# Kernel optimization log

Hardware: AMD Instinct MI355X
Metric: run time of the kernel (lower is better)

Reference implementation:

```python
import jax, jax.numpy as jnp
import numpy as np

B, T, C = 2, 192, 512
H, D = 8, 64  # num_heads, head_dim; inner_dim = H*D = C


def setup_inputs() -> dict:
    key = jax.random.key(0)
    k1, k2, k3 = jax.random.split(key, 3)
    x = jax.random.normal(k1, (B, T, C), dtype=jnp.float32)
    W_in = jax.random.normal(k2, (C, 5 * H * D), dtype=jnp.float32) * 0.02
    b_in = jnp.zeros((5 * H * D,), dtype=jnp.float32)
    W_out = jax.random.normal(k3, (H * D, C), dtype=jnp.float32) * 0.02
    b_out = jnp.zeros((C,), dtype=jnp.float32)
    return {"x": x, "W_in": W_in, "b_in": b_in, "W_out": W_out, "b_out": b_out}


def _split_heads(t):
    # (B,T,H*D) -> (B,H,T,D)
    return t.reshape(B, T, H, D).transpose(0, 2, 1, 3)


def reference(x, W_in, b_in, W_out, b_out):
    scale = D ** -0.5
    proj = x @ W_in + b_in  # (B,T,5*H*D)
    q, k1, v1, k2, v2 = jnp.split(proj, 5, axis=-1)
    q = _split_heads(q) * scale
    k1 = _split_heads(k1)
    v1 = _split_heads(v1)
    k2 = _split_heads(k2)
    v2 = _split_heads(v2)
    # trilinear logits: <q_i, k1_j, k2_k> / sqrt(D), computed in fp32
    logits = jnp.einsum('bhid,bhjd,bhkd->bhijk', q, k1, k2,
                        preferred_element_type=jnp.float32)
    # softmax over the joint (j,k) axes
    attn = jax.nn.softmax(logits.reshape(B, H, T, T * T), axis=-1)
    attn = attn.reshape(B, H, T, T, T).astype(x.dtype)
    # out_i[d] = sum_{j,k} attn[i,j,k] * v1_j[d] * v2_k[d]
    out = jnp.einsum('bhijk,bhjd,bhkd->bhid', attn, v1, v2)
    y = out.transpose(0, 2, 1, 3).reshape(B, T, H * D)  # merge heads
    return y @ W_out + b_out
```

## Files before the change

### kernel.cpp

```cpp
#include <hip/hip_runtime.h>
#include <hip/hip_bf16.h>


typedef float  v4f __attribute__((ext_vector_type(4)));
typedef short  v8s __attribute__((ext_vector_type(8)));

__device__ __forceinline__ unsigned short f2bf(float f) {
  unsigned u = __float_as_uint(f);
  u += 0x7fffu + ((u >> 16) & 1u);
  return (unsigned short)(u >> 16);
}
__device__ __forceinline__ float bf2f(unsigned short b) {
  return __uint_as_float(((unsigned)b) << 16);
}
__device__ __forceinline__ unsigned pack_bf16(float lo, float hi) {
  __hip_bfloat162 t = __float22bfloat162_rn(float2{lo, hi});
  union { __hip_bfloat162 b; unsigned u; } cv;
  cv.b = t;
  return cv.u;
}

#if __has_builtin(__builtin_amdgcn_exp2f)
#define EXP2F(x) __builtin_amdgcn_exp2f(x)
#else
#define EXP2F(x) exp2f(x)
#endif

#define MFMA32(a, b, c) __builtin_amdgcn_mfma_f32_16x16x32_bf16((a), (b), (c), 0, 0, 0)

#define QSCALE 0.18033688011112042f


#define XH_OFF   589824
#define XL_OFF   786432
#define WTH_OFF  983040
#define WTL_OFF  2293760
#define WOTH_OFF 3604480
#define WOTL_OFF 3866624
#define OH_OFF   4128768
#define OL_OFF   4325376

__device__ __forceinline__ int v1perm(int t) {
  return (t & ~31) | (((t >> 2) & 3) << 3) | ((t & 3) << 1) | ((t >> 4) & 1);
}

__global__ __launch_bounds__(256) void prep_kernel(
    const float* __restrict__ x, const float* __restrict__ Win,
    const float* __restrict__ Wout, unsigned short* __restrict__ wsh) {
  __shared__ float tile[32 * 65];
  const int bi = blockIdx.x, t = threadIdx.x;
  if (bi < 768) {
    const float* W; unsigned short *Th, *Tl; int R, n0, k0;
    if (bi < 640) {
      W = Win; Th = wsh + WTH_OFF; Tl = wsh + WTL_OFF; R = 2560;
      n0 = (bi % 40) << 6; k0 = (bi / 40) << 5;
    } else {
      const int idx = bi - 640;
      W = Wout; Th = wsh + WOTH_OFF; Tl = wsh + WOTL_OFF; R = 512;
      n0 = (idx & 7) << 6; k0 = (idx >> 3) << 5;
    }
    const int n = t & 63, kq = (t >> 6) * 8;
#pragma unroll
    for (int j = 0; j < 8; ++j)
      tile[(kq + j) * 65 + n] = W[(k0 + kq + j) * R + n0 + n];
    __syncthreads();
    const int n2 = t >> 2, ks = (t & 3) * 8;
    union { uint4 u; unsigned short us[8]; } ph, pl;
#pragma unroll
    for (int j = 0; j < 8; ++j) {
      const float v = tile[(ks + j) * 65 + n2];
      const unsigned short h = f2bf(v);
      ph.us[j] = h;
      pl.us[j] = f2bf(v - bf2f(h));
    }
    *(uint4*)(Th + (n0 + n2) * 512 + k0 + ks) = ph.u;
    *(uint4*)(Tl + (n0 + n2) * 512 + k0 + ks) = pl.u;
  } else {
    const int flat = ((bi - 768) * 256 + t) * 8;
    const v4f v0 = *(const v4f*)(x + flat);
    const v4f v1 = *(const v4f*)(x + flat + 4);
    union { uint4 u; unsigned short us[8]; } ph, pl;
#pragma unroll
    for (int j = 0; j < 4; ++j) {
      unsigned short h = f2bf(v0[j]);
      ph.us[j] = h; pl.us[j] = f2bf(v0[j] - bf2f(h));
      h = f2bf(v1[j]);
      ph.us[4 + j] = h; pl.us[4 + j] = f2bf(v1[j] - bf2f(h));
    }
    *(uint4*)(wsh + XH_OFF + flat) = ph.u;
    *(uint4*)(wsh + XL_OFF + flat) = pl.u;
  }
}

__global__ __launch_bounds__(64) void proj_kernel(
    const unsigned short* __restrict__ wsh, const float* __restrict__ bin,
    float* __restrict__ wsf, unsigned short* __restrict__ wshd) {
  const int lane = threadIdx.x;
  const int c = lane & 15, q = lane >> 4;
  const int bm = blockIdx.x % 12, bn = blockIdx.x / 12;

  const unsigned short* base[8];
  base[0] = wsh + XH_OFF + (bm * 32 + c) * 512 + (q << 3);
  base[1] = base[0] + 16 * 512;
  base[2] = wsh + XL_OFF + (bm * 32 + c) * 512 + (q << 3);
  base[3] = base[2] + 16 * 512;
  base[4] = wsh + WTH_OFF + (bn * 32 + c) * 512 + (q << 3);
  base[5] = base[4] + 16 * 512;
  base[6] = wsh + WTL_OFF + (bn * 32 + c) * 512 + (q << 3);
  base[7] = base[6] + 16 * 512;

  const v4f z = {0.f, 0.f, 0.f, 0.f};
  v4f a00 = z, a01 = z, a10 = z, a11 = z;

  v8s cur[8], nxt[8];
#pragma unroll
  for (int i = 0; i < 8; ++i) cur[i] = *(const v8s*)(base[i]);
#pragma unroll
  for (int i = 0; i < 8; ++i) nxt[i] = *(const v8s*)(base[i] + 32);

#pragma unroll 1
  for (int ks = 0; ks < 16; ++ks) {
    v8s nx2[8];
    if (ks < 14) {
      const int o = (ks + 2) * 32;
#pragma unroll
      for (int i = 0; i < 8; ++i) nx2[i] = *(const v8s*)(base[i] + o);
    }
    a00 = MFMA32(cur[2], cur[4], a00); a00 = MFMA32(cur[0], cur[6], a00); a00 = MFMA32(cur[0], cur[4], a00);
    a01 = MFMA32(cur[2], cur[5], a01); a01 = MFMA32(cur[0], cur[7], a01); a01 = MFMA32(cur[0], cur[5], a01);
    a10 = MFMA32(cur[3], cur[4], a10); a10 = MFMA32(cur[1], cur[6], a10); a10 = MFMA32(cur[1], cur[4], a10);
    a11 = MFMA32(cur[3], cur[5], a11); a11 = MFMA32(cur[1], cur[7], a11); a11 = MFMA32(cur[1], cur[5], a11);
#pragma unroll
    for (int i = 0; i < 8; ++i) { cur[i] = nxt[i]; nxt[i] = nx2[i]; }
  }

  v4f accs[2][2] = {{a00, a01}, {a10, a11}};
#pragma unroll
  for (int mt = 0; mt < 2; ++mt) {
#pragma unroll
    for (int nt = 0; nt < 2; ++nt) {
      const int n = bn * 32 + nt * 16 + c;
      const int which = n >> 9, cc = n & 511, h = cc >> 6, d = cc & 63;
      const float bv = bin[n];
#pragma unroll
      for (int r = 0; r < 4; ++r) {
        const int m = bm * 32 + mt * 16 + (q << 2) + r;
        const int b = (m >= 192) ? 1 : 0;
        const int tt = m - (b ? 192 : 0);
        const int bh = b * 8 + h;
        const float val = accs[mt][nt][r] + bv;
        const int rm = ((bh * 192 + tt) << 6) + d;
        if (which == 0)      wsf[rm] = val * QSCALE;
        else if (which == 1) wshd[rm] = f2bf(val);
        else if (which == 2) wshd[393216 + ((bh << 6) + d) * 192 + v1perm(tt)] = f2bf(val);
        else if (which == 3) wshd[196608 + rm] = f2bf(val);
        else wsf[196608 + ((bh * 192 + tt) * 16 + (d & 15)) * 4 + (d >> 4)] = val;
      }
    }
  }
}

__global__ __launch_bounds__(256, 2) void attn_kernel(
    const float* __restrict__ wsf, const unsigned short* __restrict__ wsh,
    float* __restrict__ accp, float* __restrict__ Sp) {
  __shared__ char smem[16640];
  unsigned short* K2s = (unsigned short*)smem;

  const int tid  = threadIdx.x;
  const int wv   = tid >> 6;
  const int lane = tid & 63;
  const int c    = lane & 15;
  const int quad = lane >> 4;
  const int jh   = wv & 1;
  const int kh   = wv >> 1;

  const int bb = blockIdx.x;
  const int kb = bb & 3;
  const int it = (bb >> 2) % 12;
  const int bh = bb / 48;

  const unsigned short* k1g = wsh + bh * 192 * 64;
  const unsigned short* v1g = wsh + 393216 + bh * 64 * 192;
  const unsigned short* k2g = wsh + 196608 + bh * 192 * 64;
  const float*          v2g = wsf + 196608 + bh * 12288;

  for (int idx = tid; idx < 384; idx += 256) {
    const int r = idx >> 3, c8 = (idx & 7) * 8;
    *(uint4*)(K2s + r * 64 + c8) = *(const uint4*)(k2g + (kb * 48 + r) * 64 + c8);
  }

  v8s k1f[6][2];
#pragma unroll
  for (int j = 0; j < 6; ++j) {
    const unsigned short* kp = k1g + (((jh * 6 + j) * 16 + c) << 6) + (quad << 3);
    k1f[j][0] = *(const v8s*)(kp);
    k1f[j][1] = *(const v8s*)(kp + 32);
  }

  v8s vf[3][4];
#pragma unroll
  for (int m = 0; m < 3; ++m)
#pragma unroll
    for (int t = 0; t < 4; ++t)
      vf[m][t] = *(const v8s*)(v1g + (c + 16 * t) * 192 + ((jh * 3 + m) << 5) + (quad << 3));

  const float* qg = wsf + ((bh * 192 + it * 16 + c) << 6) + (quad << 3);
  float q0[8], q1[8];
  {
    v4f qa = *(const v4f*)(qg), qb = *(const v4f*)(qg + 4);
    v4f qc = *(const v4f*)(qg + 32), qd = *(const v4f*)(qg + 36);
#pragma unroll
    for (int e = 0; e < 4; ++e) {
      q0[e] = qa[e]; q0[4 + e] = qb[e];
      q1[e] = qc[e]; q1[4 + e] = qd[e];
    }
  }
  __syncthreads();

  unsigned* Pw = (unsigned*)(smem + 6144) + wv * 320;
  const v4f z = {0.f, 0.f, 0.f, 0.f};
  v4f acc[4] = {z, z, z, z};
  v4f oS = z;
  const short one = (short)0x3F80;
  const v8s ones = {one, one, one, one, one, one, one, one};

  union U4 { uint4 u4; unsigned short us[8]; };
  union AF { v8s v; unsigned u[4]; };

#pragma unroll 1
  for (int ks = 0; ks < 24; ++ks) {
    const int rl = kh * 24 + ks;
    U4 kl, khh;
    kl.u4  = *(const uint4*)(K2s + (rl << 6) + (quad << 3));
    khh.u4 = *(const uint4*)(K2s + (rl << 6) + (quad << 3) + 32);
    const v4f v2v = *(const v4f*)(v2g + (((kb * 48 + rl) << 4) + c) * 4);

    AF af0, af1;
#pragma unroll
    for (int e = 0; e < 4; ++e) {
      af0.u[e] = pack_bf16(q0[2*e] * bf2f(kl.us[2*e]),  q0[2*e+1] * bf2f(kl.us[2*e+1]));
      af1.u[e] = pack_bf16(q1[2*e] * bf2f(khh.us[2*e]), q1[2*e+1] * bf2f(khh.us[2*e+1]));
    }

    v4f o0 = z, o1 = z, o2 = z, o3 = z;
#pragma unroll
    for (int m = 0; m < 3; ++m) {
      v4f Ca = MFMA32(af0.v, k1f[2*m][0], z);
      Ca = MFMA32(af1.v, k1f[2*m][1], Ca);
      v4f Cb = MFMA32(af0.v, k1f[2*m+1][0], z);
      Cb = MFMA32(af1.v, k1f[2*m+1][1], Cb);
#pragma unroll
      for (int r = 0; r < 4; ++r) { Ca[r] = EXP2F(Ca[r]); Cb[r] = EXP2F(Cb[r]); }
#pragma unroll
      for (int r = 0; r < 4; ++r)
        Pw[((quad << 2) + r) * 20 + c] = pack_bf16(Ca[r], Cb[r]);
      const v8s ap = *(const v8s*)(Pw + c * 20 + (quad << 2));
      oS = MFMA32(ap, ones, oS);
      o0 = MFMA32(ap, vf[m][0], o0);
      o1 = MFMA32(ap, vf[m][1], o1);
      o2 = MFMA32(ap, vf[m][2], o2);
      o3 = MFMA32(ap, vf[m][3], o3);
    }
    acc[0] += o0 * v2v[0];
    acc[1] += o1 * v2v[1];
    acc[2] += o2 * v2v[2];
    acc[3] += o3 * v2v[3];
  }

  __syncthreads();
  float* redA = (float*)smem;
  float* redS = (float*)smem + 4096;

  if (c == 0) {
    float* rs = redS + wv * 16 + (quad << 2);
#pragma unroll
    for (int r = 0; r < 4; ++r) rs[r] = oS[r];
  }
#pragma unroll
  for (int r = 0; r < 4; ++r) {
    float* rr = redA + wv * 1024 + (((quad << 2) + r) << 6) + c;
    rr[0] = acc[0][r]; rr[16] = acc[1][r]; rr[32] = acc[2][r]; rr[48] = acc[3][r];
  }
  __syncthreads();

  const int pbase = (bh * 12 + it) * 4 + kb;
  float* ap_out = accp + pbase * 1024;
  for (int idx = tid; idx < 1024; idx += 256)
    ap_out[idx] = redA[idx] + redA[1024 + idx] + redA[2048 + idx] + redA[3072 + idx];
  if (tid < 16)
    Sp[pbase * 16 + tid] = redS[tid] + redS[16 + tid] + redS[32 + tid] + redS[48 + tid];
}

__global__ __launch_bounds__(256) void norm_kernel(
    const float* __restrict__ accp, const float* __restrict__ Sp,
    unsigned short* __restrict__ wsh) {
  const int flat = blockIdx.x * 2048 + threadIdx.x * 8;
  const int m = flat >> 9, cc = flat & 511;
  const int b = (m >= 192) ? 1 : 0;
  const int tt = m - (b ? 192 : 0);
  const int h = cc >> 6, d0 = cc & 63;
  const int bh = b * 8 + h, it = tt >> 4, i = tt & 15;
  const int pb = (bh * 12 + it) * 4;
  const float* ap = accp + pb * 1024 + (i << 6) + d0;
  v4f a0 = *(const v4f*)(ap), a1 = *(const v4f*)(ap + 4);
  float Sv = Sp[pb * 16 + i];
#pragma unroll
  for (int kb = 1; kb < 4; ++kb) {
    a0 += *(const v4f*)(ap + kb * 1024);
    a1 += *(const v4f*)(ap + kb * 1024 + 4);
    Sv += Sp[(pb + kb) * 16 + i];
  }
  const float inv = 1.0f / Sv;
  union { uint4 u; unsigned short us[8]; } ph, pl;
#pragma unroll
  for (int j = 0; j < 4; ++j) {
    float v = a0[j] * inv;
    unsigned short hh = f2bf(v);
    ph.us[j] = hh; pl.us[j] = f2bf(v - bf2f(hh));
    v = a1[j] * inv;
    hh = f2bf(v);
    ph.us[4 + j] = hh; pl.us[4 + j] = f2bf(v - bf2f(hh));
  }
  *(uint4*)(wsh + OH_OFF + flat) = ph.u;
  *(uint4*)(wsh + OL_OFF + flat) = pl.u;
}

__global__ __launch_bounds__(64) void outp_kernel(
    const unsigned short* __restrict__ wsh, const float* __restrict__ bout,
    float* __restrict__ y) {
  const int lane = threadIdx.x;
  const int c = lane & 15, q = lane >> 4;
  const int bm = blockIdx.x % 12, bn = blockIdx.x / 12;

  const unsigned short* base[8];
  base[0] = wsh + OH_OFF + (bm * 32 + c) * 512 + (q << 3);
  base[1] = base[0] + 16 * 512;
  base[2] = wsh + OL_OFF + (bm * 32 + c) * 512 + (q << 3);
  base[3] = base[2] + 16 * 512;
  base[4] = wsh + WOTH_OFF + (bn * 32 + c) * 512 + (q << 3);
  base[5] = base[4] + 16 * 512;
  base[6] = wsh + WOTL_OFF + (bn * 32 + c) * 512 + (q << 3);
  base[7] = base[6] + 16 * 512;

  const v4f z = {0.f, 0.f, 0.f, 0.f};
  v4f a00 = z, a01 = z, a10 = z, a11 = z;

  v8s cur[8], nxt[8];
#pragma unroll
  for (int i = 0; i < 8; ++i) cur[i] = *(const v8s*)(base[i]);
#pragma unroll
  for (int i = 0; i < 8; ++i) nxt[i] = *(const v8s*)(base[i] + 32);

#pragma unroll 1
  for (int ks = 0; ks < 16; ++ks) {
    v8s nx2[8];
    if (ks < 14) {
      const int o = (ks + 2) * 32;
#pragma unroll
      for (int i = 0; i < 8; ++i) nx2[i] = *(const v8s*)(base[i] + o);
    }
    a00 = MFMA32(cur[2], cur[4], a00); a00 = MFMA32(cur[0], cur[6], a00); a00 = MFMA32(cur[0], cur[4], a00);
    a01 = MFMA32(cur[2], cur[5], a01); a01 = MFMA32(cur[0], cur[7], a01); a01 = MFMA32(cur[0], cur[5], a01);
    a10 = MFMA32(cur[3], cur[4], a10); a10 = MFMA32(cur[1], cur[6], a10); a10 = MFMA32(cur[1], cur[4], a10);
    a11 = MFMA32(cur[3], cur[5], a11); a11 = MFMA32(cur[1], cur[7], a11); a11 = MFMA32(cur[1], cur[5], a11);
#pragma unroll
    for (int i = 0; i < 8; ++i) { cur[i] = nxt[i]; nxt[i] = nx2[i]; }
  }

  v4f accs[2][2] = {{a00, a01}, {a10, a11}};
#pragma unroll
  for (int mt = 0; mt < 2; ++mt) {
#pragma unroll
    for (int nt = 0; nt < 2; ++nt) {
      const int n = bn * 32 + nt * 16 + c;
      const float bv = bout[n];
#pragma unroll
      for (int r = 0; r < 4; ++r) {
        const int m = bm * 32 + mt * 16 + (q << 2) + r;
        y[m * 512 + n] = accs[mt][nt][r] + bv;
      }
    }
  }
}

extern "C" void kernel_launch(void* const* d_in, const int* in_sizes, int n_in,
                              void* d_out, int out_size, void* d_ws, size_t ws_size,
                              hipStream_t stream) {
  const float* x    = (const float*)d_in[0];
  const float* Win  = (const float*)d_in[1];
  const float* bin  = (const float*)d_in[2];
  const float* Wout = (const float*)d_in[3];
  const float* bout = (const float*)d_in[4];

  float* wsf = (float*)d_ws;
  unsigned short* wsh = (unsigned short*)(wsf + 1191936);
  float* accp = wsf + 393216;
  float* Sp   = wsf + 1179648;

  prep_kernel<<<dim3(864), 256, 0, stream>>>(x, Win, Wout, wsh);
  proj_kernel<<<dim3(960), 64, 0, stream>>>(wsh, bin, wsf, wsh);
  attn_kernel<<<dim3(768), 256, 0, stream>>>(wsf, wsh, accp, Sp);
  norm_kernel<<<dim3(96), 256, 0, stream>>>(accp, Sp, wsh);
  outp_kernel<<<dim3(192), 64, 0, stream>>>(wsh, bout, (float*)d_out);
}
```

Measured before the change: 150.4 us.

## Transpose MFMA operands to keep softmax probabilities in registers

Swaps the A/B operands of the logit MFMAs so the output tile is transposed. The exponentiated probabilities can then be packed directly into the B operand of the value MFMAs, which removes the per-iteration LDS write/read round trip and its shuffle. The row-sum is now a scalar register accumulation instead of an MFMA against a ones vector, and the v1 permutation and v2 workspace layouts are changed to match the new fragment ordering. The cost is four vector loads of v2 per iteration instead of one and a larger partial-sum reduction.

```diff
diff --git a/kernel.cpp b/kernel.cpp
--- a/kernel.cpp
+++ b/kernel.cpp
@@ -41,7 +41,7 @@
 #define OL_OFF   4325376
 
 __device__ __forceinline__ int v1perm(int t) {
-  return (t & ~31) | (((t >> 2) & 3) << 3) | ((t & 3) << 1) | ((t >> 4) & 1);
+  return (t & ~31) | (((t >> 2) & 3) << 3) | (((t >> 4) & 1) << 2) | (t & 3);
 }
 
 __global__ __launch_bounds__(256) void prep_kernel(
@@ -154,7 +154,7 @@
         else if (which == 1) wshd[rm] = f2bf(val);
         else if (which == 2) wshd[393216 + ((bh << 6) + d) * 192 + v1perm(tt)] = f2bf(val);
         else if (which == 3) wshd[196608 + rm] = f2bf(val);
-        else wsf[196608 + ((bh * 192 + tt) * 16 + (d & 15)) * 4 + (d >> 4)] = val;
+        else wsf[196608 + ((bh * 192 + tt) << 6) + ((d >> 4) << 4) + (d & 15)] = val;
       }
     }
   }
@@ -163,7 +163,7 @@
 __global__ __launch_bounds__(256, 2) void attn_kernel(
     const float* __restrict__ wsf, const unsigned short* __restrict__ wsh,
     float* __restrict__ accp, float* __restrict__ Sp) {
-  __shared__ char smem[16640];
+  __shared__ char smem[17408];
   unsigned short* K2s = (unsigned short*)smem;
 
   const int tid  = threadIdx.x;
@@ -201,8 +201,8 @@
 #pragma unroll
   for (int m = 0; m < 3; ++m)
 #pragma unroll
-    for (int t = 0; t < 4; ++t)
-      vf[m][t] = *(const v8s*)(v1g + (c + 16 * t) * 192 + ((jh * 3 + m) << 5) + (quad << 3));
+    for (int dt = 0; dt < 4; ++dt)
+      vf[m][dt] = *(const v8s*)(v1g + (dt * 16 + c) * 192 + ((jh * 3 + m) << 5) + (quad << 3));
 
   const float* qg = wsf + ((bh * 192 + it * 16 + c) << 6) + (quad << 3);
   float q0[8], q1[8];
@@ -217,12 +217,9 @@
   }
   __syncthreads();
 
-  unsigned* Pw = (unsigned*)(smem + 6144) + wv * 320;
   const v4f z = {0.f, 0.f, 0.f, 0.f};
   v4f acc[4] = {z, z, z, z};
-  v4f oS = z;
-  const short one = (short)0x3F80;
-  const v8s ones = {one, one, one, one, one, one, one, one};
+  float sS = 0.f;
 
   union U4 { uint4 u4; unsigned short us[8]; };
   union AF { v8s v; unsigned u[4]; };
@@ -233,7 +230,11 @@
     U4 kl, khh;
     kl.u4  = *(const uint4*)(K2s + (rl << 6) + (quad << 3));
     khh.u4 = *(const uint4*)(K2s + (rl << 6) + (quad << 3) + 32);
-    const v4f v2v = *(const v4f*)(v2g + (((kb * 48 + rl) << 4) + c) * 4);
+    const float* vb = v2g + ((kb * 48 + rl) << 6) + (quad << 2);
+    const v4f vt0 = *(const v4f*)(vb);
+    const v4f vt1 = *(const v4f*)(vb + 16);
+    const v4f vt2 = *(const v4f*)(vb + 32);
+    const v4f vt3 = *(const v4f*)(vb + 48);
 
     AF af0, af1;
 #pragma unroll
@@ -245,50 +246,52 @@
     v4f o0 = z, o1 = z, o2 = z, o3 = z;
 #pragma unroll
     for (int m = 0; m < 3; ++m) {
-      v4f Ca = MFMA32(af0.v, k1f[2*m][0], z);
-      Ca = MFMA32(af1.v, k1f[2*m][1], Ca);
-      v4f Cb = MFMA32(af0.v, k1f[2*m+1][0], z);
-      Cb = MFMA32(af1.v, k1f[2*m+1][1], Cb);
+      v4f Ca = MFMA32(k1f[2*m][0],   af0.v, z);
+      Ca = MFMA32(k1f[2*m][1],   af1.v, Ca);
+      v4f Cb = MFMA32(k1f[2*m+1][0], af0.v, z);
+      Cb = MFMA32(k1f[2*m+1][1], af1.v, Cb);
 #pragma unroll
       for (int r = 0; r < 4; ++r) { Ca[r] = EXP2F(Ca[r]); Cb[r] = EXP2F(Cb[r]); }
-#pragma unroll
-      for (int r = 0; r < 4; ++r)
-        Pw[((quad << 2) + r) * 20 + c] = pack_bf16(Ca[r], Cb[r]);
-      const v8s ap = *(const v8s*)(Pw + c * 20 + (quad << 2));
-      oS = MFMA32(ap, ones, oS);
-      o0 = MFMA32(ap, vf[m][0], o0);
-      o1 = MFMA32(ap, vf[m][1], o1);
-      o2 = MFMA32(ap, vf[m][2], o2);
-      o3 = MFMA32(ap, vf[m][3], o3);
-    }
-    acc[0] += o0 * v2v[0];
-    acc[1] += o1 * v2v[1];
-    acc[2] += o2 * v2v[2];
-    acc[3] += o3 * v2v[3];
+      sS += Ca[0] + Ca[1] + Ca[2] + Ca[3] + Cb[0] + Cb[1] + Cb[2] + Cb[3];
+      AF pp;
+      pp.u[0] = pack_bf16(Ca[0], Ca[1]);
+      pp.u[1] = pack_bf16(Ca[2], Ca[3]);
+      pp.u[2] = pack_bf16(Cb[0], Cb[1]);
+      pp.u[3] = pack_bf16(Cb[2], Cb[3]);
+      o0 = MFMA32(vf[m][0], pp.v, o0);
+      o1 = MFMA32(vf[m][1], pp.v, o1);
+      o2 = MFMA32(vf[m][2], pp.v, o2);
+      o3 = MFMA32(vf[m][3], pp.v, o3);
+    }
+    acc[0] += o0 * vt0;
+    acc[1] += o1 * vt1;
+    acc[2] += o2 * vt2;
+    acc[3] += o3 * vt3;
   }
 
   __syncthreads();
   float* redA = (float*)smem;
   float* redS = (float*)smem + 4096;
 
-  if (c == 0) {
-    float* rs = redS + wv * 16 + (quad << 2);
-#pragma unroll
-    for (int r = 0; r < 4; ++r) rs[r] = oS[r];
-  }
-#pragma unroll
-  for (int r = 0; r < 4; ++r) {
-    float* rr = redA + wv * 1024 + (((quad << 2) + r) << 6) + c;
-    rr[0] = acc[0][r]; rr[16] = acc[1][r]; rr[32] = acc[2][r]; rr[48] = acc[3][r];
-  }
+#pragma unroll
+  for (int dt = 0; dt < 4; ++dt)
+    *(v4f*)(redA + wv * 1024 + (c << 6) + (dt << 4) + (quad << 2)) = acc[dt];
+  redS[wv * 64 + (quad << 4) + c] = sS;
   __syncthreads();
 
   const int pbase = (bh * 12 + it) * 4 + kb;
   float* ap_out = accp + pbase * 1024;
   for (int idx = tid; idx < 1024; idx += 256)
     ap_out[idx] = redA[idx] + redA[1024 + idx] + redA[2048 + idx] + redA[3072 + idx];
-  if (tid < 16)
-    Sp[pbase * 16 + tid] = redS[tid] + redS[16 + tid] + redS[32 + tid] + redS[48 + tid];
+  if (tid < 16) {
+    float s = 0.f;
+#pragma unroll
+    for (int w = 0; w < 4; ++w)
+#pragma unroll
+      for (int qq = 0; qq < 4; ++qq)
+        s += redS[w * 64 + qq * 16 + tid];
+    Sp[pbase * 16 + tid] = s;
+  }
 }
 
 __global__ __launch_bounds__(256) void norm_kernel(
```

Result: faster. 143.8 us (-4.4%).
